# Optimization experiments

Measured on AMD Instinct MI355X. Metric: run time of the kernel, lower is better.

Reference implementation:

```python
import jax, jax.numpy as jnp
import numpy as np

NUM_HEADS = 12


def get_rel_pos(q_size, k_size, rel_pos):
    # relative coordinate lookup (q_size == k_size here; table has 2*size >= 2*size-1 rows)
    idx = jnp.arange(q_size)[:, None] - jnp.arange(k_size)[None, :] + (k_size - 1)
    return rel_pos[idx]  # [q_size, k_size, head_dim]


def setup_inputs() -> dict:
    key = jax.random.key(0)
    ks = jax.random.split(key, 5)
    B, H, W, E = 8, 32, 32, 768
    hd = E // NUM_HEADS
    x = jax.random.normal(ks[0], (B, H, W, E), jnp.float32)
    Wqkv = jax.random.normal(ks[1], (E, 3 * E), jnp.float32) * (E ** -0.5)
    bqkv = jnp.zeros((3 * E,), jnp.float32)
    Wproj = jax.random.normal(ks[2], (E, E), jnp.float32) * (E ** -0.5)
    bproj = jnp.zeros((E,), jnp.float32)
    rel_pos_h = jax.random.normal(ks[3], (2 * H, hd), jnp.float32) * 0.02
    rel_pos_w = jax.random.normal(ks[4], (2 * W, hd), jnp.float32) * 0.02
    return dict(x=x, Wqkv=Wqkv, bqkv=bqkv, Wproj=Wproj, bproj=bproj,
                rel_pos_h=rel_pos_h, rel_pos_w=rel_pos_w)


def reference(x, Wqkv, bqkv, Wproj, bproj, rel_pos_h, rel_pos_w):
    B, H, W, E = x.shape
    nh = NUM_HEADS
    hd = E // nh
    N = H * W
    scale = hd ** -0.5
    # QKV projection, then the exact reshape/transpose sequence of the TF module
    qkv = x.reshape(B, N, E) @ Wqkv + bqkv                       # [B, N, 3E]
    qkv = qkv.reshape(B, N, nh, hd, 3).transpose(0, 1, 2, 4, 3)  # [B, N, nh, 3, hd]
    qkv = qkv.reshape(B * nh, N, hd, 3)                          # raw row-major reshape (faithful)
    q, k, v = qkv[..., 0], qkv[..., 1], qkv[..., 2]              # each [B*nh, N, hd]
    attn = jnp.einsum('bnd,bmd->bnm', q * scale, k)              # [B*nh, N, N]
    # decomposed relative position bias (SAM-style)
    Rh = get_rel_pos(H, H, rel_pos_h)                            # [H, H, hd]
    Rw = get_rel_pos(W, W, rel_pos_w)                            # [W, W, hd]
    r_q = q.reshape(B * nh, H, W, hd)
    rel_h = jnp.einsum('bhwc,hkc->bhwk', r_q, Rh)                # [B*nh, H, W, H]
    rel_w = jnp.einsum('bhwc,wkc->bhwk', r_q, Rw)                # [B*nh, H, W, W]
    attn = (attn.reshape(B * nh, H, W, H, W)
            + rel_h[..., :, None]
            + rel_w[..., None, :]).reshape(B * nh, N, N)
    attn = jax.nn.softmax(attn, axis=-1)
    out = attn @ v                                               # [B*nh, N, hd]
    # faithful raw reshape + transpose back to [B, H, W, E]
    out = out.reshape(B, H, W, nh, hd).transpose(0, 3, 1, 2, 4).reshape(B, H, W, nh * hd)
    return out @ Wproj + bproj
```

## Files before the change

kernel.cpp:

```cpp
#include <hip/hip_runtime.h>
#include <hip/hip_bf16.h>


typedef __attribute__((ext_vector_type(8))) short short8;
typedef __attribute__((ext_vector_type(4))) float f32x4;

__global__ __launch_bounds__(256) void cast_f32_bf16(const float* __restrict__ in,
                                                     __hip_bfloat16* __restrict__ out) {
  int i = (blockIdx.x * 256 + threadIdx.x) * 4;
  float4 v = *(const float4*)&in[i];
  out[i + 0] = __float2bfloat16(v.x);
  out[i + 1] = __float2bfloat16(v.y);
  out[i + 2] = __float2bfloat16(v.z);
  out[i + 3] = __float2bfloat16(v.w);
}

__global__ __launch_bounds__(256) void transpose_cast(const float* __restrict__ in,
                                                      __hip_bfloat16* __restrict__ out,
                                                      int K, int N) {
  __shared__ float tile[32][33];
  int n0 = blockIdx.x * 32, k0 = blockIdx.y * 32;
  int tx = threadIdx.x & 31, ty = threadIdx.x >> 5;
#pragma unroll
  for (int i = 0; i < 4; ++i)
    tile[ty + i * 8][tx] = in[(size_t)(k0 + ty + i * 8) * N + n0 + tx];
  __syncthreads();
#pragma unroll
  for (int i = 0; i < 4; ++i)
    out[(size_t)(n0 + ty + i * 8) * K + k0 + tx] = __float2bfloat16(tile[tx][ty + i * 8]);
}

__device__ inline void gload16(const void* g, void* l) {
  __builtin_amdgcn_global_load_lds((const __attribute__((address_space(1))) void*)g,
                                   (__attribute__((address_space(3))) void*)l, 16, 0, 0);
}

template<int BM, bool OUT_BF16>
__global__ __launch_bounds__(256) void gemm_dma(const __hip_bfloat16* __restrict__ A,
                                                const __hip_bfloat16* __restrict__ Bt,
                                                const float* __restrict__ bias,
                                                void* __restrict__ Cout,
                                                int N, int K) {
  constexpr int FM = BM / 32;
  __shared__ __hip_bfloat16 Al[BM * 64];
  __shared__ __hip_bfloat16 Bl[128 * 64];
  int n0 = blockIdx.x * 128, m0 = blockIdx.y * BM;
  int tid = threadIdx.x, lane = tid & 63, wid = tid >> 6;
  int wm = wid >> 1, wn = wid & 1;
  int lr = lane & 15, lg = lane >> 4;
  int row_l = lane >> 3, col8 = (lane & 7) * 8;
  f32x4 acc[FM][4] = {};
  for (int k0 = 0; k0 < K; k0 += 64) {
#pragma unroll
    for (int j = 0; j < BM / 32; ++j) {
      int jj = wid * (BM / 32) + j;
      int arow = jj * 8 + row_l;
      gload16(&A[(size_t)(m0 + arow) * K + k0 + col8], &Al[jj * 512]);
    }
#pragma unroll
    for (int j = 0; j < 4; ++j) {
      int jj = wid * 4 + j;
      int brow = jj * 8 + row_l;
      gload16(&Bt[(size_t)(n0 + brow) * K + k0 + col8], &Bl[jj * 512]);
    }
    __syncthreads();
#pragma unroll
    for (int ks = 0; ks < 2; ++ks) {
      short8 af[FM], bfr[4];
#pragma unroll
      for (int m = 0; m < FM; ++m)
        af[m] = *(const short8*)&Al[(wm * (BM / 2) + m * 16 + lr) * 64 + ks * 32 + lg * 8];
#pragma unroll
      for (int n = 0; n < 4; ++n)
        bfr[n] = *(const short8*)&Bl[(wn * 64 + n * 16 + lr) * 64 + ks * 32 + lg * 8];
#pragma unroll
      for (int m = 0; m < FM; ++m)
#pragma unroll
        for (int n = 0; n < 4; ++n)
          acc[m][n] = __builtin_amdgcn_mfma_f32_16x16x32_bf16(af[m], bfr[n], acc[m][n], 0, 0, 0);
    }
    __syncthreads();
  }
#pragma unroll
  for (int n = 0; n < 4; ++n) {
    int col = n0 + wn * 64 + n * 16 + lr;
    float bv = bias[col];
#pragma unroll
    for (int m = 0; m < FM; ++m) {
      int rowb = m0 + wm * (BM / 2) + m * 16 + lg * 4;
#pragma unroll
      for (int r = 0; r < 4; ++r) {
        float v = acc[m][n][r] + bv;
        if (OUT_BF16)
          ((__hip_bfloat16*)Cout)[(size_t)(rowb + r) * N + col] = __float2bfloat16(v);
        else
          ((float*)Cout)[(size_t)(rowb + r) * N + col] = v;
      }
    }
  }
}

__global__ __launch_bounds__(256) void permute_v2(const __hip_bfloat16* __restrict__ qkv,
                                                  __hip_bfloat16* __restrict__ Q,
                                                  __hip_bfloat16* __restrict__ Kd,
                                                  __hip_bfloat16* __restrict__ Vt) {
  int bh = blockIdx.y, n0 = blockIdx.x * 64;
  int tid = threadIdx.x;
  __shared__ short raw[64 * 200];
  __shared__ short vt[64][72];
  const short* src = (const short*)qkv + (size_t)(bh * 1024 + n0) * 192;
#pragma unroll
  for (int i = 0; i < 6; ++i) {
    int c16 = tid + i * 256;
    int wi = c16 / 24, off = (c16 % 24) * 8;
    *(short8*)&raw[wi * 200 + off] = *(const short8*)&src[(size_t)c16 * 8];
  }
  __syncthreads();
  int wi = tid >> 2, g4 = tid & 3;
  const short* rw_ = &raw[wi * 200];
  short8 qv[2], kv_[2];
#pragma unroll
  for (int half = 0; half < 2; ++half)
#pragma unroll
    for (int j = 0; j < 8; ++j) {
      int d2 = g4 * 16 + half * 8 + j;
      int u = 3 * d2;
      qv[half][j]  = rw_[((u) & 63) * 3 + ((u) >> 6)];
      kv_[half][j] = rw_[((u + 1) & 63) * 3 + ((u + 1) >> 6)];
      vt[d2][wi]   = rw_[((u + 2) & 63) * 3 + ((u + 2) >> 6)];
    }
  size_t base = (size_t)bh * 65536 + (size_t)(n0 + wi) * 64 + g4 * 16;
  *(short8*)&Q[base] = qv[0];
  *(short8*)&Q[base + 8] = qv[1];
  *(short8*)&Kd[base] = kv_[0];
  *(short8*)&Kd[base + 8] = kv_[1];
  __syncthreads();
  int d2r = tid >> 2;
  size_t vbase = (size_t)bh * 65536 + (size_t)d2r * 1024 + n0 + g4 * 16;
  *(short8*)&Vt[vbase]     = *(const short8*)&vt[d2r][g4 * 16];
  *(short8*)&Vt[vbase + 8] = *(const short8*)&vt[d2r][g4 * 16 + 8];
}

__device__ inline short8 cvt8(const float* p) {
  short8 r;
#pragma unroll
  for (int j = 0; j < 8; ++j) {
    __hip_bfloat16 b = __float2bfloat16(p[j]);
    r[j] = *reinterpret_cast<const short*>(&b);
  }
  return r;
}

__device__ inline unsigned packtrunc(float a, float b) {
  return __builtin_amdgcn_perm(__float_as_uint(b), __float_as_uint(a), 0x07060302u);
}

#define L2E 1.44269504088896f
__global__ __launch_bounds__(256) void attn10(const __hip_bfloat16* __restrict__ Q,
                                              const __hip_bfloat16* __restrict__ Kd,
                                              const __hip_bfloat16* __restrict__ Vt,
                                              const float* __restrict__ rph,
                                              const float* __restrict__ rpw,
                                              __hip_bfloat16* __restrict__ outp) {
  int orig = blockIdx.x;
  int xcd = orig & 7, loc = orig >> 3;
  int bh = xcd * 12 + (loc % 12);
  int qt = loc / 12;
  int tid = threadIdx.x;
  int lane = tid & 63, w = tid >> 6;
  int lr = lane & 15, lg = lane >> 4;
  int xr = lr & 7;

  __shared__ __hip_bfloat16 Kl[2][4096];
  __shared__ __hip_bfloat16 Vl[2][4096];
  __shared__ __hip_bfloat16 rh_b[4][32 * 36];
  __shared__ __align__(16) char scratch[4][2304];

  const __hip_bfloat16* Qb = Q + (size_t)bh * 65536;
  const __hip_bfloat16* Kb = Kd + (size_t)bh * 65536;
  const __hip_bfloat16* Vb = Vt + (size_t)bh * 65536;

  int q0 = qt * 128 + w * 32;
  int hq = q0 >> 5;

  short8 qf[2][2];
#pragma unroll
  for (int qh = 0; qh < 2; ++qh) {
    qf[qh][0] = *(const short8*)&Qb[(size_t)(q0 + qh * 16 + lr) * 64 + lg * 8];
    qf[qh][1] = *(const short8*)&Qb[(size_t)(q0 + qh * 16 + lr) * 64 + 32 + lg * 8];
  }

  __hip_bfloat16* rhw = rh_b[w];
#pragma unroll
  for (int kt = 0; kt < 2; ++kt) {
    int row = hq - (kt * 16 + lr) + 31;
    const float* tp = rph + (size_t)row * 64 + lg * 8;
    short8 th0 = cvt8(tp), th1 = cvt8(tp + 32);
#pragma unroll
    for (int qh = 0; qh < 2; ++qh) {
      f32x4 a = {};
      a = __builtin_amdgcn_mfma_f32_16x16x32_bf16(qf[qh][0], th0, a, 0, 0, 0);
      a = __builtin_amdgcn_mfma_f32_16x16x32_bf16(qf[qh][1], th1, a, 0, 0, 0);
#pragma unroll
      for (int r = 0; r < 4; ++r)
        rhw[(qh * 16 + lg * 4 + r) * 36 + kt * 16 + lr] = __float2bfloat16(a[r] * L2E);
    }
  }
  __hip_bfloat16* rwt = (w < 2) ? ((__hip_bfloat16*)Kl + w * 2176)
                                : ((__hip_bfloat16*)Vl + (w - 2) * 2176);
#pragma unroll
  for (int jt = 0; jt < 4; ++jt) {
    const float* tp = rpw + (size_t)(jt * 16 + lr) * 64 + lg * 8;
    short8 tw0 = cvt8(tp), tw1 = cvt8(tp + 32);
#pragma unroll
    for (int qh = 0; qh < 2; ++qh) {
      f32x4 a = {};
      a = __builtin_amdgcn_mfma_f32_16x16x32_bf16(qf[qh][0], tw0, a, 0, 0, 0);
      a = __builtin_amdgcn_mfma_f32_16x16x32_bf16(qf[qh][1], tw1, a, 0, 0, 0);
#pragma unroll
      for (int r = 0; r < 4; ++r)
        rwt[(qh * 16 + lg * 4 + r) * 68 + jt * 16 + lr] = __float2bfloat16(a[r] * L2E);
    }
  }
  float rwreg[2][8];
#pragma unroll
  for (int qh = 0; qh < 2; ++qh) {
    int wq = qh * 16 + lr;
#pragma unroll
    for (int i = 0; i < 8; ++i) {
      int k = (i >> 2) * 16 + lg * 4 + (i & 3);
      rwreg[qh][i] = __bfloat162float(rwt[(qh * 16 + lr) * 68 + (wq - k + 31)]);
    }
  }
  __syncthreads();

  f32x4 O[2][4] = {};
  float m_[2] = {-1e30f, -1e30f};
  float lsum[2] = {0.f, 0.f};
  const float C = 0.125f * L2E;
  char* pc = scratch[w];

  int g_ = lane >> 3;
  int colb = ((lane & 7) ^ g_) * 8;

#pragma unroll
  for (int i = 0; i < 2; ++i) {
    int op = 2 * w + i;
    gload16(&Kb[(size_t)(op * 8 + g_) * 64 + colb], &Kl[0][op * 512]);
    gload16(&Vb[(size_t)(op * 8 + g_) * 1024 + colb], &Vl[0][op * 512]);
  }

  int cur = 0;
#pragma unroll 1
  for (int kv0 = 0; kv0 < 1024; kv0 += 64) {
    __builtin_amdgcn_s_barrier();
    int nkv = (kv0 + 64 < 1024) ? kv0 + 64 : 960;
#pragma unroll
    for (int i = 0; i < 2; ++i) {
      int op = 2 * w + i;
      gload16(&Kb[(size_t)(nkv + op * 8 + g_) * 64 + colb], &Kl[cur ^ 1][op * 512]);
      gload16(&Vb[(size_t)(op * 8 + g_) * 1024 + nkv + colb], &Vl[cur ^ 1][op * 512]);
    }
    asm volatile("s_waitcnt vmcnt(4)" ::: "memory");
    __builtin_amdgcn_sched_barrier(0);
    __builtin_amdgcn_s_barrier();
    __builtin_amdgcn_sched_barrier(0);

    const char* kc = (const char*)Kl[cur];
    const char* vc = (const char*)Vl[cur];
    short8 kf[8];
#pragma unroll
    for (int t = 0; t < 4; ++t)
#pragma unroll
      for (int h = 0; h < 2; ++h)
        kf[2 * t + h] = *(const short8*)(kc + (t * 16 + lr) * 128 + (((h * 4 + lg) ^ xr) * 16));
    f32x4 st[2][4];
#pragma unroll
    for (int t = 0; t < 4; ++t)
#pragma unroll
      for (int qh = 0; qh < 2; ++qh) {
        f32x4 z = {};
        z = __builtin_amdgcn_mfma_f32_16x16x32_bf16(kf[2 * t], qf[qh][0], z, 0, 0, 0);
        z = __builtin_amdgcn_mfma_f32_16x16x32_bf16(kf[2 * t + 1], qf[qh][1], z, 0, 0, 0);
        st[qh][t] = z;
      }
    int kh = kv0 >> 5;
    float mxl[2];
#pragma unroll
    for (int qh = 0; qh < 2; ++qh) {
      float bh0 = __bfloat162float(rhw[(qh * 16 + lr) * 36 + kh]);
      float bh1 = __bfloat162float(rhw[(qh * 16 + lr) * 36 + kh + 1]);
      float mx = -1e30f;
#pragma unroll
      for (int t = 0; t < 4; ++t)
#pragma unroll
        for (int r = 0; r < 4; ++r) {
          float sv = fmaf(st[qh][t][r], C, ((t < 2) ? bh0 : bh1) + rwreg[qh][(t & 1) * 4 + r]);
          st[qh][t][r] = sv;
          mx = fmaxf(mx, sv);
        }
      mxl[qh] = mx;
    }
    int cond = (mxl[0] <= m_[0] + 8.f) && (mxl[1] <= m_[1] + 8.f);
    if (!__all(cond)) {
#pragma unroll
      for (int qh = 0; qh < 2; ++qh) {
        float mw = fmaxf(mxl[qh], __shfl_xor(mxl[qh], 16, 64));
        mw = fmaxf(mw, __shfl_xor(mw, 32, 64));
        float mnew = fmaxf(m_[qh], mw);
        float al = exp2f(m_[qh] - mnew);
        lsum[qh] *= al;
        m_[qh] = mnew;
#pragma unroll
        for (int r = 0; r < 4; ++r) {
          float av = __shfl(al, lg * 4 + r, 64);
#pragma unroll
          for (int dt = 0; dt < 4; ++dt) O[qh][dt][r] *= av;
        }
      }
    }
    short8 pf[2][2];
#pragma unroll
    for (int qh = 0; qh < 2; ++qh) {
      float mq = m_[qh];
      float sa = 0.f;
#pragma unroll
      for (int t = 0; t < 4; ++t) {
        float p0 = exp2f(st[qh][t][0] - mq);
        float p1 = exp2f(st[qh][t][1] - mq);
        float p2 = exp2f(st[qh][t][2] - mq);
        float p3 = exp2f(st[qh][t][3] - mq);
        sa += (p0 + p1) + (p2 + p3);
        uint2 wv;
        wv.x = packtrunc(p0, p1);
        wv.y = packtrunc(p2, p3);
        int slot = (2 * t + (lg >> 1)) ^ xr;
        *(uint2*)(pc + lr * 128 + slot * 16 + (lg & 1) * 8) = wv;
      }
      lsum[qh] += sa;
      pf[qh][0] = *(const short8*)(pc + lr * 128 + (((0 + lg) ^ xr) * 16));
      pf[qh][1] = *(const short8*)(pc + lr * 128 + (((4 + lg) ^ xr) * 16));
    }
#pragma unroll
    for (int dt = 0; dt < 4; ++dt) {
      short8 vf0 = *(const short8*)(vc + (dt * 16 + lr) * 128 + (((0 + lg) ^ xr) * 16));
      short8 vf1 = *(const short8*)(vc + (dt * 16 + lr) * 128 + (((4 + lg) ^ xr) * 16));
#pragma unroll
      for (int qh = 0; qh < 2; ++qh) {
        O[qh][dt] = __builtin_amdgcn_mfma_f32_16x16x32_bf16(pf[qh][0], vf0, O[qh][dt], 0, 0, 0);
        O[qh][dt] = __builtin_amdgcn_mfma_f32_16x16x32_bf16(pf[qh][1], vf1, O[qh][dt], 0, 0, 0);
      }
    }
    cur ^= 1;
  }

#pragma unroll
  for (int qh = 0; qh < 2; ++qh) {
    float lt = lsum[qh];
    lt += __shfl_xor(lt, 16, 64);
    lt += __shfl_xor(lt, 32, 64);
    float linv = 1.f / lt;
#pragma unroll
    for (int r = 0; r < 4; ++r) {
      float lv = __shfl(linv, lg * 4 + r, 64);
      int n = q0 + qh * 16 + lg * 4 + r;
#pragma unroll
      for (int dt = 0; dt < 4; ++dt) {
        int d = dt * 16 + lr;
        int Sidx = bh * 65536 + n * 64 + d;
        int b = Sidx / 786432, r1 = Sidx % 786432;
        int pp = r1 / 24576, r2 = r1 % 24576;
        int qq = r2 / 768, r3 = r2 % 768;
        int j = r3 >> 6, dd = r3 & 63;
        int P = b * 786432 + j * 65536 + pp * 2048 + qq * 64 + dd;
        outp[P] = __float2bfloat16(O[qh][dt][r] * lv);
      }
    }
  }
}

extern "C" void kernel_launch(void* const* d_in, const int* in_sizes, int n_in,
                              void* d_out, int out_size, void* d_ws, size_t ws_size,
                              hipStream_t stream) {
  const float* x     = (const float*)d_in[0];
  const float* Wqkv  = (const float*)d_in[1];
  const float* bqkv  = (const float*)d_in[2];
  const float* Wproj = (const float*)d_in[3];
  const float* bproj = (const float*)d_in[4];
  const float* rph   = (const float*)d_in[5];
  const float* rpw   = (const float*)d_in[6];
  float* out = (float*)d_out;
  char* ws = (char*)d_ws;

  __hip_bfloat16* xb     = (__hip_bfloat16*)(ws);
  __hip_bfloat16* wqkvT  = (__hip_bfloat16*)(ws + 12582912);
  __hip_bfloat16* wprojT = (__hip_bfloat16*)(ws + 16121856);
  __hip_bfloat16* qkvb   = (__hip_bfloat16*)(ws + 17301504);
  __hip_bfloat16* Qm     = (__hip_bfloat16*)(ws + 55050240);
  __hip_bfloat16* Km     = (__hip_bfloat16*)(ws + 67633152);
  __hip_bfloat16* Vtm    = (__hip_bfloat16*)(ws + 80216064);

  cast_f32_bf16<<<dim3(6144), dim3(256), 0, stream>>>(x, xb);
  transpose_cast<<<dim3(72, 24), dim3(256), 0, stream>>>(Wqkv, wqkvT, 768, 2304);
  transpose_cast<<<dim3(24, 24), dim3(256), 0, stream>>>(Wproj, wprojT, 768, 768);
  gemm_dma<128, true><<<dim3(18, 64), dim3(256), 0, stream>>>(xb, wqkvT, bqkv, (void*)qkvb, 2304, 768);
  permute_v2<<<dim3(16, 96), dim3(256), 0, stream>>>(qkvb, Qm, Km, Vtm);
  attn10<<<dim3(768), dim3(256), 0, stream>>>(Qm, Km, Vtm, rph, rpw, qkvb);
  gemm_dma<64, false><<<dim3(6, 128), dim3(256), 0, stream>>>(qkvb, wprojT, bproj, (void*)out, 768, 768);
}
```

Baseline: 182.1 us.

## Shrink attention LDS footprint by single-buffering V and packing scratch regions

Merges the attention kernel's shared arrays into one 40 KB buffer. V is now single-buffered and loaded within the same iteration, guarded by an extra wait and barrier before the P·V MFMAs. The relative-height bias table is repacked so both bias values come from one 32-bit load, and launch bounds request four blocks per CU. This trades exposed V load latency and an extra barrier for lower LDS use and potentially higher occupancy.

```diff
diff --git a/kernel.cpp b/kernel.cpp
--- a/kernel.cpp
+++ b/kernel.cpp
@@ -156,12 +156,12 @@
 }
 
 #define L2E 1.44269504088896f
-__global__ __launch_bounds__(256) void attn10(const __hip_bfloat16* __restrict__ Q,
-                                              const __hip_bfloat16* __restrict__ Kd,
-                                              const __hip_bfloat16* __restrict__ Vt,
-                                              const float* __restrict__ rph,
-                                              const float* __restrict__ rpw,
-                                              __hip_bfloat16* __restrict__ outp) {
+__global__ __launch_bounds__(256, 4) void attn11(const __hip_bfloat16* __restrict__ Q,
+                                                 const __hip_bfloat16* __restrict__ Kd,
+                                                 const __hip_bfloat16* __restrict__ Vt,
+                                                 const float* __restrict__ rph,
+                                                 const float* __restrict__ rpw,
+                                                 __hip_bfloat16* __restrict__ outp) {
   int orig = blockIdx.x;
   int xcd = orig & 7, loc = orig >> 3;
   int bh = xcd * 12 + (loc % 12);
@@ -171,10 +171,7 @@
   int lr = lane & 15, lg = lane >> 4;
   int xr = lr & 7;
 
-  __shared__ __hip_bfloat16 Kl[2][4096];
-  __shared__ __hip_bfloat16 Vl[2][4096];
-  __shared__ __hip_bfloat16 rh_b[4][32 * 36];
-  __shared__ __align__(16) char scratch[4][2304];
+  __shared__ __align__(16) char lds[40960];
 
   const __hip_bfloat16* Qb = Q + (size_t)bh * 65536;
   const __hip_bfloat16* Kb = Kd + (size_t)bh * 65536;
@@ -190,7 +187,7 @@
     qf[qh][1] = *(const short8*)&Qb[(size_t)(q0 + qh * 16 + lr) * 64 + 32 + lg * 8];
   }
 
-  __hip_bfloat16* rhw = rh_b[w];
+  __hip_bfloat16* rhw = (__hip_bfloat16*)(lds + 24576 + w * 2048);
 #pragma unroll
   for (int kt = 0; kt < 2; ++kt) {
     int row = hq - (kt * 16 + lr) + 31;
@@ -203,11 +200,10 @@
       a = __builtin_amdgcn_mfma_f32_16x16x32_bf16(qf[qh][1], th1, a, 0, 0, 0);
 #pragma unroll
       for (int r = 0; r < 4; ++r)
-        rhw[(qh * 16 + lg * 4 + r) * 36 + kt * 16 + lr] = __float2bfloat16(a[r] * L2E);
-    }
-  }
-  __hip_bfloat16* rwt = (w < 2) ? ((__hip_bfloat16*)Kl + w * 2176)
-                                : ((__hip_bfloat16*)Vl + (w - 2) * 2176);
+        rhw[(qh * 16 + lg * 4 + r) * 32 + kt * 16 + lr] = __float2bfloat16(a[r] * L2E);
+    }
+  }
+  __hip_bfloat16* rwt = (__hip_bfloat16*)(lds + w * 4352);
 #pragma unroll
   for (int jt = 0; jt < 4; ++jt) {
     const float* tp = rpw + (size_t)(jt * 16 + lr) * 64 + lg * 8;
@@ -238,7 +234,8 @@
   float m_[2] = {-1e30f, -1e30f};
   float lsum[2] = {0.f, 0.f};
   const float C = 0.125f * L2E;
-  char* pc = scratch[w];
+  char* pc = lds + 32768 + w * 2048;
+  char* vcb = lds + 16384;
 
   int g_ = lane >> 3;
   int colb = ((lane & 7) ^ g_) * 8;
@@ -246,28 +243,31 @@
 #pragma unroll
   for (int i = 0; i < 2; ++i) {
     int op = 2 * w + i;
-    gload16(&Kb[(size_t)(op * 8 + g_) * 64 + colb], &Kl[0][op * 512]);
-    gload16(&Vb[(size_t)(op * 8 + g_) * 1024 + colb], &Vl[0][op * 512]);
+    gload16(&Kb[(size_t)(op * 8 + g_) * 64 + colb], lds + op * 1024);
   }
 
   int cur = 0;
 #pragma unroll 1
   for (int kv0 = 0; kv0 < 1024; kv0 += 64) {
+    __builtin_amdgcn_sched_barrier(0);
     __builtin_amdgcn_s_barrier();
-    int nkv = (kv0 + 64 < 1024) ? kv0 + 64 : 960;
 #pragma unroll
     for (int i = 0; i < 2; ++i) {
       int op = 2 * w + i;
-      gload16(&Kb[(size_t)(nkv + op * 8 + g_) * 64 + colb], &Kl[cur ^ 1][op * 512]);
-      gload16(&Vb[(size_t)(op * 8 + g_) * 1024 + nkv + colb], &Vl[cur ^ 1][op * 512]);
+      gload16(&Vb[(size_t)(op * 8 + g_) * 1024 + kv0 + colb], vcb + op * 1024);
+    }
+    int nkv = (kv0 + 64 < 1024) ? kv0 + 64 : 960;
+#pragma unroll
+    for (int i = 0; i < 2; ++i) {
+      int op = 2 * w + i;
+      gload16(&Kb[(size_t)(nkv + op * 8 + g_) * 64 + colb], lds + (cur ^ 1) * 8192 + op * 1024);
     }
     asm volatile("s_waitcnt vmcnt(4)" ::: "memory");
     __builtin_amdgcn_sched_barrier(0);
     __builtin_amdgcn_s_barrier();
     __builtin_amdgcn_sched_barrier(0);
 
-    const char* kc = (const char*)Kl[cur];
-    const char* vc = (const char*)Vl[cur];
+    const char* kc = lds + cur * 8192;
     short8 kf[8];
 #pragma unroll
     for (int t = 0; t < 4; ++t)
@@ -284,12 +284,12 @@
         z = __builtin_amdgcn_mfma_f32_16x16x32_bf16(kf[2 * t + 1], qf[qh][1], z, 0, 0, 0);
         st[qh][t] = z;
       }
-    int kh = kv0 >> 5;
     float mxl[2];
 #pragma unroll
     for (int qh = 0; qh < 2; ++qh) {
-      float bh0 = __bfloat162float(rhw[(qh * 16 + lr) * 36 + kh]);
-      float bh1 = __bfloat162float(rhw[(qh * 16 + lr) * 36 + kh + 1]);
+      unsigned bu = *(const unsigned*)(lds + 24576 + w * 2048 + (qh * 16 + lr) * 64 + (kv0 >> 4));
+      float bh0 = __uint_as_float(bu << 16);
+      float bh1 = __uint_as_float(bu & 0xffff0000u);
       float mx = -1e30f;
 #pragma unroll
       for (int t = 0; t < 4; ++t)
@@ -341,10 +341,14 @@
       pf[qh][0] = *(const short8*)(pc + lr * 128 + (((0 + lg) ^ xr) * 16));
       pf[qh][1] = *(const short8*)(pc + lr * 128 + (((4 + lg) ^ xr) * 16));
     }
+    asm volatile("s_waitcnt vmcnt(2)" ::: "memory");
+    __builtin_amdgcn_sched_barrier(0);
+    __builtin_amdgcn_s_barrier();
+    __builtin_amdgcn_sched_barrier(0);
 #pragma unroll
     for (int dt = 0; dt < 4; ++dt) {
-      short8 vf0 = *(const short8*)(vc + (dt * 16 + lr) * 128 + (((0 + lg) ^ xr) * 16));
-      short8 vf1 = *(const short8*)(vc + (dt * 16 + lr) * 128 + (((4 + lg) ^ xr) * 16));
+      short8 vf0 = *(const short8*)(vcb + (dt * 16 + lr) * 128 + (((0 + lg) ^ xr) * 16));
+      short8 vf1 = *(const short8*)(vcb + (dt * 16 + lr) * 128 + (((4 + lg) ^ xr) * 16));
 #pragma unroll
       for (int qh = 0; qh < 2; ++qh) {
         O[qh][dt] = __builtin_amdgcn_mfma_f32_16x16x32_bf16(pf[qh][0], vf0, O[qh][dt], 0, 0, 0);
@@ -405,6 +409,6 @@
   transpose_cast<<<dim3(24, 24), dim3(256), 0, stream>>>(Wproj, wprojT, 768, 768);
   gemm_dma<128, true><<<dim3(18, 64), dim3(256), 0, stream>>>(xb, wqkvT, bqkv, (void*)qkvb, 2304, 768);
   permute_v2<<<dim3(16, 96), dim3(256), 0, stream>>>(qkvb, Qm, Km, Vtm);
-  attn10<<<dim3(768), dim3(256), 0, stream>>>(Qm, Km, Vtm, rph, rpw, qkvb);
+  attn11<<<dim3(768), dim3(256), 0, stream>>>(Qm, Km, Vtm, rph, rpw, qkvb);
   gemm_dma<64, false><<<dim3(6, 128), dim3(256), 0, stream>>>(qkvb, wprojT, bproj, (void*)out, 768, 768);
 }
```

Measured after the change: 180.1 us. About the same (-1.1%).
